# Performance work log

Hardware: AMD Instinct MI355X
Metric: run time of the kernel (lower is better)

## Reference

```python
import jax, jax.numpy as jnp
import numpy as np

N_NODES = 200000
INPUT_DIM = 128
HIDDEN_DIM = 128
NUM_WALKS = 16384   # total walks across the batch of graphs
WALK_LEN = 20


def setup_inputs() -> dict:
    key = jax.random.key(0)
    ks = jax.random.split(key, 6)
    s_in = 1.0 / np.sqrt(INPUT_DIM)
    s_h = 1.0 / np.sqrt(HIDDEN_DIM)
    return {
        "x": jax.random.normal(ks[0], (N_NODES, INPUT_DIM), dtype=jnp.float32),
        "walks": jax.random.randint(ks[1], (NUM_WALKS, WALK_LEN), 0, N_NODES),
        "W_f": jax.random.normal(ks[2], (HIDDEN_DIM, INPUT_DIM), dtype=jnp.float32) * s_in,
        "b_f": jnp.zeros((HIDDEN_DIM,), dtype=jnp.float32),
        "W_ih": jax.random.normal(ks[3], (3 * HIDDEN_DIM, HIDDEN_DIM), dtype=jnp.float32) * s_h,
        "W_hh": jax.random.normal(ks[4], (3 * HIDDEN_DIM, HIDDEN_DIM), dtype=jnp.float32) * s_h,
        "b_ih": jnp.zeros((3 * HIDDEN_DIM,), dtype=jnp.float32),
        "b_hh": jnp.zeros((3 * HIDDEN_DIM,), dtype=jnp.float32),
    }


def _gru_final(seq, W_ih, W_hh, b_ih, b_hh):
    # seq: [B, T, H]; torch GRU gate order: reset, update, new. Returns final h: [B, H].
    B = seq.shape[0]
    H = W_hh.shape[1]

    def step(h, x_t):
        gx = x_t @ W_ih.T + b_ih            # [B, 3H]
        gh = h @ W_hh.T + b_hh              # [B, 3H]
        xr, xz, xn = jnp.split(gx, 3, axis=-1)
        hr, hz, hn = jnp.split(gh, 3, axis=-1)
        r = jax.nn.sigmoid(xr + hr)
        z = jax.nn.sigmoid(xz + hz)
        n = jnp.tanh(xn + r * hn)
        h_new = (1.0 - z) * n + z * h
        return h_new, None

    h0 = jnp.zeros((B, H), dtype=seq.dtype)
    h_final, _ = jax.lax.scan(step, h0, jnp.swapaxes(seq, 0, 1))  # scan over time
    return h_final


def reference(x, walks, W_f, b_f, W_ih, W_hh, b_ih, b_hh):
    # feature_encoder: Linear(input_dim -> hidden_dim)
    x_encoded = x @ W_f.T + b_f             # [N, H]
    # vectorized replacement of the scalar double-loop gather
    walk_features = x_encoded[walks]        # [B, T, H]
    path_encodings = _gru_final(walk_features, W_ih, W_hh, b_ih, b_hh)  # [B, H]
    return path_encodings
```

## Files before the change

### kernel.cpp

```cpp
#include <hip/hip_runtime.h>
#include <cstddef>

#define NWALKS 16384
#define TLEN   20
#define HDIM   128
#define WPB    32
#define NTHR   512

typedef __attribute__((ext_vector_type(8))) _Float16 f16x8;
typedef __attribute__((ext_vector_type(4))) _Float16 f16x4;
typedef __attribute__((ext_vector_type(2))) __fp16   h16x2;
typedef __attribute__((ext_vector_type(4))) float    f32x4;

union H4 { f16x4 v; struct { h16x2 lo, hi; } p; };

__global__ void fold_kernel(const float* __restrict__ W_f, const float* __restrict__ b_f,
                            const float* __restrict__ W_ih, const float* __restrict__ W_hh,
                            const float* __restrict__ b_ih,
                            _Float16* __restrict__ Wc16, _Float16* __restrict__ Whh16,
                            float* __restrict__ b_c) {
  const int r = blockIdx.x;
  const int i = threadIdx.x;
  const float scale = (r < 256) ? -1.4426950408889634f : 2.8853900817779268f;
  const float* wih = W_ih + r * HDIM;
  float acc = 0.f;
  for (int h = 0; h < HDIM; ++h) acc = fmaf(wih[h], W_f[h * HDIM + i], acc);
  Wc16[r * HDIM + i]  = (_Float16)(acc * scale);
  Whh16[r * HDIM + i] = (_Float16)(W_hh[r * HDIM + i] * scale);
  if (i == 0) {
    float bb = b_ih[r];
    for (int h = 0; h < HDIM; ++h) bb = fmaf(wih[h], b_f[h], bb);
    b_c[r] = bb;
  }
}

__global__ __launch_bounds__(NTHR, 2)
void gru_kernel(const float* __restrict__ x, const int* __restrict__ walks,
                const _Float16* __restrict__ Wc16, const _Float16* __restrict__ Whh16,
                const float* __restrict__ b_c, const float* __restrict__ b_hh,
                float* __restrict__ out) {
  __shared__ _Float16 hbuf[2][WPB][HDIM];
  __shared__ _Float16 xbuf[2][WPB][HDIM];
  __shared__ int      nodes[TLEN][WPB];

  const int tid  = threadIdx.x;
  const int lane = tid & 63;
  const int wv   = tid >> 6;
  const int g    = lane >> 4;
  const int l15  = lane & 15;
  const int jw   = wv * 16 + l15;
  const int j0   = wv * 16 + 4 * g;
  const int walk0 = blockIdx.x * WPB;

  for (int idx = tid; idx < TLEN * WPB; idx += NTHR)
    nodes[idx >> 5][idx & 31] = walks[(walk0 + (idx & 31)) * TLEN + (idx >> 5)];
  for (int idx = tid; idx < WPB * HDIM; idx += NTHR)
    hbuf[0][0][idx] = (_Float16)0.f;

  f16x8 wrx[4], wrh[4], wzx[4], wzh[4], wnx[4], wnh[4];
#pragma unroll
  for (int kt = 0; kt < 4; ++kt) {
    const int koff = kt * 32 + g * 8;
    wrx[kt] = *(const f16x8*)(Wc16  + (size_t)(jw)       * HDIM + koff);
    wzx[kt] = *(const f16x8*)(Wc16  + (size_t)(128 + jw) * HDIM + koff);
    wnx[kt] = *(const f16x8*)(Wc16  + (size_t)(256 + jw) * HDIM + koff);
    wrh[kt] = *(const f16x8*)(Whh16 + (size_t)(jw)       * HDIM + koff);
    wzh[kt] = *(const f16x8*)(Whh16 + (size_t)(128 + jw) * HDIM + koff);
    wnh[kt] = *(const f16x8*)(Whh16 + (size_t)(256 + jw) * HDIM + koff);
  }
  const float NEG_L2E = -1.4426950408889634f;
  const float TWO_L2E =  2.8853900817779268f;
  const f32x4 br4  = NEG_L2E * (*(const f32x4*)&b_c[j0]       + *(const f32x4*)&b_hh[j0]);
  const f32x4 bz4  = NEG_L2E * (*(const f32x4*)&b_c[128 + j0] + *(const f32x4*)&b_hh[128 + j0]);
  const f32x4 bxn4 = TWO_L2E * (*(const f32x4*)&b_c[256 + j0]);
  const f32x4 bhn4 = TWO_L2E * (*(const f32x4*)&b_hh[256 + j0]);

  f32x4 hprev[2];
  hprev[0] = 0.f; hprev[1] = 0.f;

  int voffs[4];
#pragma unroll
  for (int kt = 0; kt < 4; ++kt)
    voffs[kt] = l15 * HDIM + ((((kt * 4 + g) ^ (l15 & 7))) << 3);
  const int srow = tid >> 4;
  const int sc   = tid & 15;
  const int xw   = srow * HDIM + ((sc ^ (srow & 7)) << 3);
  const int hw   = l15 * HDIM + (((2 * wv + (g >> 1)) ^ (l15 & 7)) << 3) + ((g & 1) << 2);

  __syncthreads();

  {
    const unsigned off0 = ((unsigned)nodes[0][srow] << 7) + sc * 8u;
    const f32x4 a = *(const f32x4*)(x + off0);
    const f32x4 b = *(const f32x4*)(x + off0 + 4);
    H4 lo, hi;
    lo.p.lo = __builtin_amdgcn_cvt_pkrtz(a.x, a.y);
    lo.p.hi = __builtin_amdgcn_cvt_pkrtz(a.z, a.w);
    hi.p.lo = __builtin_amdgcn_cvt_pkrtz(b.x, b.y);
    hi.p.hi = __builtin_amdgcn_cvt_pkrtz(b.z, b.w);
    *(f16x4*)(&xbuf[0][0][0] + xw)     = lo.v;
    *(f16x4*)(&xbuf[0][0][0] + xw + 4) = hi.v;
  }
  f32x4 PA0, PA1, PB0, PB1;
  {
    const unsigned off1 = ((unsigned)nodes[1][srow] << 7) + sc * 8u;
    PA0 = *(const f32x4*)(x + off1);
    PA1 = *(const f32x4*)(x + off1 + 4);
  }
  __syncthreads();

#define STEP(T, CUR, NXT, P0, P1, N0, N1)                                         \
  {                                                                               \
                             \
    const int tn = ((T) + 2 < TLEN) ? (T) + 2 : TLEN - 1;                         \
    const unsigned offn = ((unsigned)nodes[tn][srow] << 7) + sc * 8u;             \
    N0 = *(const f32x4*)(x + offn);                                               \
    N1 = *(const f32x4*)(x + offn + 4);                                           \
                                      \
    const _Float16* xb = &xbuf[CUR][0][0];                                        \
    const _Float16* hb = &hbuf[CUR][0][0];                                        \
    f32x4 ar[2], az[2], an[2], ah2[2];                                            \
    __builtin_amdgcn_s_setprio(1);                                                \
    _Pragma("unroll")                                                             \
    for (int kt = 0; kt < 4; ++kt) {                                              \
      const f16x8 ax0 = *(const f16x8*)(xb + voffs[kt]);                          \
      const f16x8 ax1 = *(const f16x8*)(xb + voffs[kt] + 16 * HDIM);              \
      const f16x8 ah0 = *(const f16x8*)(hb + voffs[kt]);                          \
      const f16x8 ah1 = *(const f16x8*)(hb + voffs[kt] + 16 * HDIM);              \
      ar[0]  = __builtin_amdgcn_mfma_f32_16x16x32_f16(wrx[kt], ax0, kt ? ar[0]  : br4,  0,0,0); \
      ar[1]  = __builtin_amdgcn_mfma_f32_16x16x32_f16(wrx[kt], ax1, kt ? ar[1]  : br4,  0,0,0); \
      ar[0]  = __builtin_amdgcn_mfma_f32_16x16x32_f16(wrh[kt], ah0, ar[0],  0,0,0); \
      ar[1]  = __builtin_amdgcn_mfma_f32_16x16x32_f16(wrh[kt], ah1, ar[1],  0,0,0); \
      az[0]  = __builtin_amdgcn_mfma_f32_16x16x32_f16(wzx[kt], ax0, kt ? az[0]  : bz4,  0,0,0); \
      az[1]  = __builtin_amdgcn_mfma_f32_16x16x32_f16(wzx[kt], ax1, kt ? az[1]  : bz4,  0,0,0); \
      az[0]  = __builtin_amdgcn_mfma_f32_16x16x32_f16(wzh[kt], ah0, az[0],  0,0,0); \
      az[1]  = __builtin_amdgcn_mfma_f32_16x16x32_f16(wzh[kt], ah1, az[1],  0,0,0); \
      an[0]  = __builtin_amdgcn_mfma_f32_16x16x32_f16(wnx[kt], ax0, kt ? an[0]  : bxn4, 0,0,0); \
      an[1]  = __builtin_amdgcn_mfma_f32_16x16x32_f16(wnx[kt], ax1, kt ? an[1]  : bxn4, 0,0,0); \
      ah2[0] = __builtin_amdgcn_mfma_f32_16x16x32_f16(wnh[kt], ah0, kt ? ah2[0] : bhn4, 0,0,0); \
      ah2[1] = __builtin_amdgcn_mfma_f32_16x16x32_f16(wnh[kt], ah1, kt ? ah2[1] : bhn4, 0,0,0); \
    }                                                                             \
    __builtin_amdgcn_s_setprio(0);                                                \
                    \
    {                                                                             \
      H4 lo, hi;                                                                  \
      lo.p.lo = __builtin_amdgcn_cvt_pkrtz(P0.x, P0.y);                           \
      lo.p.hi = __builtin_amdgcn_cvt_pkrtz(P0.z, P0.w);                           \
      hi.p.lo = __builtin_amdgcn_cvt_pkrtz(P1.x, P1.y);                           \
      hi.p.hi = __builtin_amdgcn_cvt_pkrtz(P1.z, P1.w);                           \
      *(f16x4*)(&xbuf[NXT][0][0] + xw)     = lo.v;                                \
      *(f16x4*)(&xbuf[NXT][0][0] + xw + 4) = hi.v;                                \
    }                                                                             \
                \
    _Pragma("unroll")                                                             \
    for (int mt = 0; mt < 2; ++mt) {                                              \
      f32x4 hn;                                                                   \
      _Pragma("unroll")                                                           \
      for (int r = 0; r < 4; ++r) {                                               \
        const float rv = __builtin_amdgcn_rcpf(1.f + __builtin_amdgcn_exp2f(ar[mt][r])); \
        const float zv = __builtin_amdgcn_rcpf(1.f + __builtin_amdgcn_exp2f(az[mt][r])); \
        const float en = __builtin_amdgcn_exp2f(fmaf(rv, ah2[mt][r], an[mt][r])); \
        const float nv = fmaf(-2.f, __builtin_amdgcn_rcpf(en + 1.f), 1.f);        \
        hn[r] = fmaf(zv, hprev[mt][r] - nv, nv);                                  \
      }                                                                           \
      hprev[mt] = hn;                                                             \
      H4 hp;                                                                      \
      hp.p.lo = __builtin_amdgcn_cvt_pkrtz(hn[0], hn[1]);                         \
      hp.p.hi = __builtin_amdgcn_cvt_pkrtz(hn[2], hn[3]);                         \
      *(f16x4*)(&hbuf[NXT][0][0] + hw + mt * 16 * HDIM) = hp.v;                   \
    }                                                                             \
    __syncthreads();                                                              \
  }

#pragma unroll 1
  for (int tt = 0; tt < TLEN; tt += 2) {
    STEP(tt,     0, 1, PA0, PA1, PB0, PB1)
    STEP(tt + 1, 1, 0, PB0, PB1, PA0, PA1)
  }
#undef STEP

#pragma unroll
  for (int mt = 0; mt < 2; ++mt) {
    float4 o = make_float4(hprev[mt][0], hprev[mt][1], hprev[mt][2], hprev[mt][3]);
    *(float4*)&out[(size_t)(walk0 + mt * 16 + l15) * HDIM + j0] = o;
  }
}

extern "C" void kernel_launch(void* const* d_in, const int* in_sizes, int n_in,
                              void* d_out, int out_size, void* d_ws, size_t ws_size,
                              hipStream_t stream) {
  const float* x     = (const float*)d_in[0];
  const int*   walks = (const int*)  d_in[1];
  const float* W_f   = (const float*)d_in[2];
  const float* b_f   = (const float*)d_in[3];
  const float* W_ih  = (const float*)d_in[4];
  const float* W_hh  = (const float*)d_in[5];
  const float* b_ih  = (const float*)d_in[6];
  const float* b_hh  = (const float*)d_in[7];
  float* out = (float*)d_out;

  _Float16* Wc16  = (_Float16*)d_ws;
  _Float16* Whh16 = Wc16 + 384 * HDIM;
  float*    b_c   = (float*)(Whh16 + 384 * HDIM);

  fold_kernel<<<3 * HDIM, HDIM, 0, stream>>>(W_f, b_f, W_ih, W_hh, b_ih, Wc16, Whh16, b_c);
  gru_kernel<<<NWALKS / WPB, NTHR, 0, stream>>>(x, walks, Wc16, Whh16, b_c, b_hh, out);
}
```

Baseline: 83.87 us.

## Software-pipeline GRU input projection one timestep ahead of recurrent matmul

The input-side gate projections (W_ih·x) for step t+1 are now computed during step t, after the recurrent h-projection MFMAs, and carried in registers. The critical dependent chain per step then holds only the h-side MFMAs followed by the gate math. The x prefetch distance grows to three steps, and a prologue computes step 0's x projection. This adds accumulator registers, which may raise register pressure and lower occupancy.

```diff
diff --git a/kernel.cpp b/kernel.cpp
--- a/kernel.cpp
+++ b/kernel.cpp
@@ -109,57 +109,91 @@
   }
   __syncthreads();
 
-#define STEP(T, CUR, NXT, P0, P1, N0, N1)                                         \
+  f32x4 PXRa[2], PXZa[2], PXNa[2], PXRb[2], PXZb[2], PXNb[2];
+  {
+    const _Float16* xb = &xbuf[0][0][0];
+#pragma unroll
+    for (int kt = 0; kt < 4; ++kt) {
+      const f16x8 ax0 = *(const f16x8*)(xb + voffs[kt]);
+      const f16x8 ax1 = *(const f16x8*)(xb + voffs[kt] + 16 * HDIM);
+      PXRa[0] = __builtin_amdgcn_mfma_f32_16x16x32_f16(wrx[kt], ax0, kt ? PXRa[0] : br4,  0,0,0);
+      PXRa[1] = __builtin_amdgcn_mfma_f32_16x16x32_f16(wrx[kt], ax1, kt ? PXRa[1] : br4,  0,0,0);
+      PXZa[0] = __builtin_amdgcn_mfma_f32_16x16x32_f16(wzx[kt], ax0, kt ? PXZa[0] : bz4,  0,0,0);
+      PXZa[1] = __builtin_amdgcn_mfma_f32_16x16x32_f16(wzx[kt], ax1, kt ? PXZa[1] : bz4,  0,0,0);
+      PXNa[0] = __builtin_amdgcn_mfma_f32_16x16x32_f16(wnx[kt], ax0, kt ? PXNa[0] : bxn4, 0,0,0);
+      PXNa[1] = __builtin_amdgcn_mfma_f32_16x16x32_f16(wnx[kt], ax1, kt ? PXNa[1] : bxn4, 0,0,0);
+    }
+  }
+  {
+    H4 lo, hi;
+    lo.p.lo = __builtin_amdgcn_cvt_pkrtz(PA0.x, PA0.y);
+    lo.p.hi = __builtin_amdgcn_cvt_pkrtz(PA0.z, PA0.w);
+    hi.p.lo = __builtin_amdgcn_cvt_pkrtz(PA1.x, PA1.y);
+    hi.p.hi = __builtin_amdgcn_cvt_pkrtz(PA1.z, PA1.w);
+    *(f16x4*)(&xbuf[1][0][0] + xw)     = lo.v;
+    *(f16x4*)(&xbuf[1][0][0] + xw + 4) = hi.v;
+  }
+  {
+    const unsigned off2 = ((unsigned)nodes[2][srow] << 7) + sc * 8u;
+    PB0 = *(const f32x4*)(x + off2);
+    PB1 = *(const f32x4*)(x + off2 + 4);
+  }
+  __syncthreads();
+
+#define STEP(T, XRD, XWR, HRD, HWR, L0, L1, S0, S1, PXR, PXZ, PXN, QXR, QXZ, QXN) \
   {                                                                               \
-                             \
-    const int tn = ((T) + 2 < TLEN) ? (T) + 2 : TLEN - 1;                         \
+    const int tn = ((T) + 3 < TLEN) ? (T) + 3 : TLEN - 1;                         \
     const unsigned offn = ((unsigned)nodes[tn][srow] << 7) + sc * 8u;             \
-    N0 = *(const f32x4*)(x + offn);                                               \
-    N1 = *(const f32x4*)(x + offn + 4);                                           \
-                                      \
-    const _Float16* xb = &xbuf[CUR][0][0];                                        \
-    const _Float16* hb = &hbuf[CUR][0][0];                                        \
-    f32x4 ar[2], az[2], an[2], ah2[2];                                            \
+    L0 = *(const f32x4*)(x + offn);                                               \
+    L1 = *(const f32x4*)(x + offn + 4);                                           \
+    const _Float16* xb = &xbuf[XRD][0][0];                                        \
+    const _Float16* hb = &hbuf[HRD][0][0];                                        \
+    f32x4 ah2[2];                                                                 \
     __builtin_amdgcn_s_setprio(1);                                                \
+              \
+    _Pragma("unroll")                                                             \
+    for (int kt = 0; kt < 4; ++kt) {                                              \
+      const f16x8 ah0 = *(const f16x8*)(hb + voffs[kt]);                          \
+      const f16x8 ah1 = *(const f16x8*)(hb + voffs[kt] + 16 * HDIM);              \
+      PXR[0] = __builtin_amdgcn_mfma_f32_16x16x32_f16(wrh[kt], ah0, PXR[0], 0,0,0); \
+      PXR[1] = __builtin_amdgcn_mfma_f32_16x16x32_f16(wrh[kt], ah1, PXR[1], 0,0,0); \
+      PXZ[0] = __builtin_amdgcn_mfma_f32_16x16x32_f16(wzh[kt], ah0, PXZ[0], 0,0,0); \
+      PXZ[1] = __builtin_amdgcn_mfma_f32_16x16x32_f16(wzh[kt], ah1, PXZ[1], 0,0,0); \
+      ah2[0] = __builtin_amdgcn_mfma_f32_16x16x32_f16(wnh[kt], ah0, kt ? ah2[0] : bhn4, 0,0,0); \
+      ah2[1] = __builtin_amdgcn_mfma_f32_16x16x32_f16(wnh[kt], ah1, kt ? ah2[1] : bhn4, 0,0,0); \
+    }                                                                             \
+                    \
     _Pragma("unroll")                                                             \
     for (int kt = 0; kt < 4; ++kt) {                                              \
       const f16x8 ax0 = *(const f16x8*)(xb + voffs[kt]);                          \
       const f16x8 ax1 = *(const f16x8*)(xb + voffs[kt] + 16 * HDIM);              \
-      const f16x8 ah0 = *(const f16x8*)(hb + voffs[kt]);                          \
-      const f16x8 ah1 = *(const f16x8*)(hb + voffs[kt] + 16 * HDIM);              \
-      ar[0]  = __builtin_amdgcn_mfma_f32_16x16x32_f16(wrx[kt], ax0, kt ? ar[0]  : br4,  0,0,0); \
-      ar[1]  = __builtin_amdgcn_mfma_f32_16x16x32_f16(wrx[kt], ax1, kt ? ar[1]  : br4,  0,0,0); \
-      ar[0]  = __builtin_amdgcn_mfma_f32_16x16x32_f16(wrh[kt], ah0, ar[0],  0,0,0); \
-      ar[1]  = __builtin_amdgcn_mfma_f32_16x16x32_f16(wrh[kt], ah1, ar[1],  0,0,0); \
-      az[0]  = __builtin_amdgcn_mfma_f32_16x16x32_f16(wzx[kt], ax0, kt ? az[0]  : bz4,  0,0,0); \
-      az[1]  = __builtin_amdgcn_mfma_f32_16x16x32_f16(wzx[kt], ax1, kt ? az[1]  : bz4,  0,0,0); \
-      az[0]  = __builtin_amdgcn_mfma_f32_16x16x32_f16(wzh[kt], ah0, az[0],  0,0,0); \
-      az[1]  = __builtin_amdgcn_mfma_f32_16x16x32_f16(wzh[kt], ah1, az[1],  0,0,0); \
-      an[0]  = __builtin_amdgcn_mfma_f32_16x16x32_f16(wnx[kt], ax0, kt ? an[0]  : bxn4, 0,0,0); \
-      an[1]  = __builtin_amdgcn_mfma_f32_16x16x32_f16(wnx[kt], ax1, kt ? an[1]  : bxn4, 0,0,0); \
-      ah2[0] = __builtin_amdgcn_mfma_f32_16x16x32_f16(wnh[kt], ah0, kt ? ah2[0] : bhn4, 0,0,0); \
-      ah2[1] = __builtin_amdgcn_mfma_f32_16x16x32_f16(wnh[kt], ah1, kt ? ah2[1] : bhn4, 0,0,0); \
+      QXR[0] = __builtin_amdgcn_mfma_f32_16x16x32_f16(wrx[kt], ax0, kt ? QXR[0] : br4,  0,0,0); \
+      QXR[1] = __builtin_amdgcn_mfma_f32_16x16x32_f16(wrx[kt], ax1, kt ? QXR[1] : br4,  0,0,0); \
+      QXZ[0] = __builtin_amdgcn_mfma_f32_16x16x32_f16(wzx[kt], ax0, kt ? QXZ[0] : bz4,  0,0,0); \
+      QXZ[1] = __builtin_amdgcn_mfma_f32_16x16x32_f16(wzx[kt], ax1, kt ? QXZ[1] : bz4,  0,0,0); \
+      QXN[0] = __builtin_amdgcn_mfma_f32_16x16x32_f16(wnx[kt], ax0, kt ? QXN[0] : bxn4, 0,0,0); \
+      QXN[1] = __builtin_amdgcn_mfma_f32_16x16x32_f16(wnx[kt], ax1, kt ? QXN[1] : bxn4, 0,0,0); \
     }                                                                             \
     __builtin_amdgcn_s_setprio(0);                                                \
-                    \
+                                                 \
     {                                                                             \
       H4 lo, hi;                                                                  \
-      lo.p.lo = __builtin_amdgcn_cvt_pkrtz(P0.x, P0.y);                           \
-      lo.p.hi = __builtin_amdgcn_cvt_pkrtz(P0.z, P0.w);                           \
-      hi.p.lo = __builtin_amdgcn_cvt_pkrtz(P1.x, P1.y);                           \
-      hi.p.hi = __builtin_amdgcn_cvt_pkrtz(P1.z, P1.w);                           \
-      *(f16x4*)(&xbuf[NXT][0][0] + xw)     = lo.v;                                \
-      *(f16x4*)(&xbuf[NXT][0][0] + xw + 4) = hi.v;                                \
-    }                                                                             \
-                \
+      lo.p.lo = __builtin_amdgcn_cvt_pkrtz(S0.x, S0.y);                           \
+      lo.p.hi = __builtin_amdgcn_cvt_pkrtz(S0.z, S0.w);                           \
+      hi.p.lo = __builtin_amdgcn_cvt_pkrtz(S1.x, S1.y);                           \
+      hi.p.hi = __builtin_amdgcn_cvt_pkrtz(S1.z, S1.w);                           \
+      *(f16x4*)(&xbuf[XWR][0][0] + xw)     = lo.v;                                \
+      *(f16x4*)(&xbuf[XWR][0][0] + xw + 4) = hi.v;                                \
+    }                                                                             \
+                                            \
     _Pragma("unroll")                                                             \
     for (int mt = 0; mt < 2; ++mt) {                                              \
       f32x4 hn;                                                                   \
       _Pragma("unroll")                                                           \
       for (int r = 0; r < 4; ++r) {                                               \
-        const float rv = __builtin_amdgcn_rcpf(1.f + __builtin_amdgcn_exp2f(ar[mt][r])); \
-        const float zv = __builtin_amdgcn_rcpf(1.f + __builtin_amdgcn_exp2f(az[mt][r])); \
-        const float en = __builtin_amdgcn_exp2f(fmaf(rv, ah2[mt][r], an[mt][r])); \
+        const float rv = __builtin_amdgcn_rcpf(1.f + __builtin_amdgcn_exp2f(PXR[mt][r])); \
+        const float zv = __builtin_amdgcn_rcpf(1.f + __builtin_amdgcn_exp2f(PXZ[mt][r])); \
+        const float en = __builtin_amdgcn_exp2f(fmaf(rv, ah2[mt][r], PXN[mt][r])); \
         const float nv = fmaf(-2.f, __builtin_amdgcn_rcpf(en + 1.f), 1.f);        \
         hn[r] = fmaf(zv, hprev[mt][r] - nv, nv);                                  \
       }                                                                           \
@@ -167,15 +201,15 @@
       H4 hp;                                                                      \
       hp.p.lo = __builtin_amdgcn_cvt_pkrtz(hn[0], hn[1]);                         \
       hp.p.hi = __builtin_amdgcn_cvt_pkrtz(hn[2], hn[3]);                         \
-      *(f16x4*)(&hbuf[NXT][0][0] + hw + mt * 16 * HDIM) = hp.v;                   \
+      *(f16x4*)(&hbuf[HWR][0][0] + hw + mt * 16 * HDIM) = hp.v;                   \
     }                                                                             \
     __syncthreads();                                                              \
   }
 
 #pragma unroll 1
   for (int tt = 0; tt < TLEN; tt += 2) {
-    STEP(tt,     0, 1, PA0, PA1, PB0, PB1)
-    STEP(tt + 1, 1, 0, PB0, PB1, PA0, PA1)
+    STEP(tt,     1, 0, 0, 1, PA0, PA1, PB0, PB1, PXRa, PXZa, PXNa, PXRb, PXZb, PXNb)
+    STEP(tt + 1, 0, 1, 1, 0, PB0, PB1, PA0, PA1, PXRb, PXZb, PXNb, PXRa, PXZa, PXNa)
   }
 #undef STEP
 
```

Result: slower. 87.19 us (+4.0%).

## Halve walks per block to 16 and replace syncthreads with LDS-only barrier

Applied to the files above, without the earlier changes.

Cuts walks per block from 32 to 16, so each wave handles one 16-walk MFMA tile per step instead of two. The gather, the LDS staging, the accumulators and the output write are reworked for the smaller tile. This doubles the grid to 1024 blocks and lowers register and LDS use per block, aiming for more blocks resident at once to hide gather latency and the serial recurrence. The per-step __syncthreads is replaced by an lgkmcnt wait plus s_barrier, so the outstanding global prefetch is no longer drained at each step. The cost is that every block reloads the weights into registers and each wave has less MFMA work to cover latency.

```diff
diff --git a/kernel.cpp b/kernel.cpp
--- a/kernel.cpp
+++ b/kernel.cpp
@@ -4,7 +4,7 @@
 #define NWALKS 16384
 #define TLEN   20
 #define HDIM   128
-#define WPB    32
+#define WPB    16
 #define NTHR   512
 
 typedef __attribute__((ext_vector_type(8))) _Float16 f16x8;
@@ -53,7 +53,7 @@
   const int walk0 = blockIdx.x * WPB;
 
   for (int idx = tid; idx < TLEN * WPB; idx += NTHR)
-    nodes[idx >> 5][idx & 31] = walks[(walk0 + (idx & 31)) * TLEN + (idx >> 5)];
+    nodes[idx >> 4][idx & 15] = walks[(walk0 + (idx & 15)) * TLEN + (idx >> 4)];
   for (int idx = tid; idx < WPB * HDIM; idx += NTHR)
     hbuf[0][0][idx] = (_Float16)0.f;
 
@@ -75,114 +75,99 @@
   const f32x4 bxn4 = TWO_L2E * (*(const f32x4*)&b_c[256 + j0]);
   const f32x4 bhn4 = TWO_L2E * (*(const f32x4*)&b_hh[256 + j0]);
 
-  f32x4 hprev[2];
-  hprev[0] = 0.f; hprev[1] = 0.f;
+  f32x4 hprev;
+  hprev = 0.f;
 
   int voffs[4];
 #pragma unroll
   for (int kt = 0; kt < 4; ++kt)
     voffs[kt] = l15 * HDIM + ((((kt * 4 + g) ^ (l15 & 7))) << 3);
-  const int srow = tid >> 4;
-  const int sc   = tid & 15;
-  const int xw   = srow * HDIM + ((sc ^ (srow & 7)) << 3);
+  const int srow = tid >> 5;
+  const int sc4  = tid & 31;
+  const int xw   = srow * HDIM + (((sc4 >> 1) ^ (srow & 7)) << 3) + ((sc4 & 1) << 2);
   const int hw   = l15 * HDIM + (((2 * wv + (g >> 1)) ^ (l15 & 7)) << 3) + ((g & 1) << 2);
 
   __syncthreads();
 
   {
-    const unsigned off0 = ((unsigned)nodes[0][srow] << 7) + sc * 8u;
+    const unsigned off0 = ((unsigned)nodes[0][srow] << 7) + sc4 * 4u;
     const f32x4 a = *(const f32x4*)(x + off0);
-    const f32x4 b = *(const f32x4*)(x + off0 + 4);
-    H4 lo, hi;
-    lo.p.lo = __builtin_amdgcn_cvt_pkrtz(a.x, a.y);
-    lo.p.hi = __builtin_amdgcn_cvt_pkrtz(a.z, a.w);
-    hi.p.lo = __builtin_amdgcn_cvt_pkrtz(b.x, b.y);
-    hi.p.hi = __builtin_amdgcn_cvt_pkrtz(b.z, b.w);
-    *(f16x4*)(&xbuf[0][0][0] + xw)     = lo.v;
-    *(f16x4*)(&xbuf[0][0][0] + xw + 4) = hi.v;
+    H4 v;
+    v.p.lo = __builtin_amdgcn_cvt_pkrtz(a.x, a.y);
+    v.p.hi = __builtin_amdgcn_cvt_pkrtz(a.z, a.w);
+    *(f16x4*)(&xbuf[0][0][0] + xw) = v.v;
   }
-  f32x4 PA0, PA1, PB0, PB1;
+  f32x4 PA, PB;
   {
-    const unsigned off1 = ((unsigned)nodes[1][srow] << 7) + sc * 8u;
-    PA0 = *(const f32x4*)(x + off1);
-    PA1 = *(const f32x4*)(x + off1 + 4);
+    const unsigned off1 = ((unsigned)nodes[1][srow] << 7) + sc4 * 4u;
+    PA = *(const f32x4*)(x + off1);
   }
   __syncthreads();
 
-#define STEP(T, CUR, NXT, P0, P1, N0, N1)                                         \
+#define STEP(T, CUR, NXT, P, N)                                                   \
   {                                                                               \
-                             \
+          \
     const int tn = ((T) + 2 < TLEN) ? (T) + 2 : TLEN - 1;                         \
-    const unsigned offn = ((unsigned)nodes[tn][srow] << 7) + sc * 8u;             \
-    N0 = *(const f32x4*)(x + offn);                                               \
-    N1 = *(const f32x4*)(x + offn + 4);                                           \
-                                      \
+    const unsigned offn = ((unsigned)nodes[tn][srow] << 7) + sc4 * 4u;            \
+    N = *(const f32x4*)(x + offn);                                                \
+                                   \
     const _Float16* xb = &xbuf[CUR][0][0];                                        \
     const _Float16* hb = &hbuf[CUR][0][0];                                        \
-    f32x4 ar[2], az[2], an[2], ah2[2];                                            \
+    f32x4 ar, az, an, ah2;                                                        \
     __builtin_amdgcn_s_setprio(1);                                                \
     _Pragma("unroll")                                                             \
     for (int kt = 0; kt < 4; ++kt) {                                              \
-      const f16x8 ax0 = *(const f16x8*)(xb + voffs[kt]);                          \
-      const f16x8 ax1 = *(const f16x8*)(xb + voffs[kt] + 16 * HDIM);              \
-      const f16x8 ah0 = *(const f16x8*)(hb + voffs[kt]);                          \
-      const f16x8 ah1 = *(const f16x8*)(hb + voffs[kt] + 16 * HDIM);              \
-      ar[0]  = __builtin_amdgcn_mfma_f32_16x16x32_f16(wrx[kt], ax0, kt ? ar[0]  : br4,  0,0,0); \
-      ar[1]  = __builtin_amdgcn_mfma_f32_16x16x32_f16(wrx[kt], ax1, kt ? ar[1]  : br4,  0,0,0); \
-      ar[0]  = __builtin_amdgcn_mfma_f32_16x16x32_f16(wrh[kt], ah0, ar[0],  0,0,0); \
-      ar[1]  = __builtin_amdgcn_mfma_f32_16x16x32_f16(wrh[kt], ah1, ar[1],  0,0,0); \
-      az[0]  = __builtin_amdgcn_mfma_f32_16x16x32_f16(wzx[kt], ax0, kt ? az[0]  : bz4,  0,0,0); \
-      az[1]  = __builtin_amdgcn_mfma_f32_16x16x32_f16(wzx[kt], ax1, kt ? az[1]  : bz4,  0,0,0); \
-      az[0]  = __builtin_amdgcn_mfma_f32_16x16x32_f16(wzh[kt], ah0, az[0],  0,0,0); \
-      az[1]  = __builtin_amdgcn_mfma_f32_16x16x32_f16(wzh[kt], ah1, az[1],  0,0,0); \
-      an[0]  = __builtin_amdgcn_mfma_f32_16x16x32_f16(wnx[kt], ax0, kt ? an[0]  : bxn4, 0,0,0); \
-      an[1]  = __builtin_amdgcn_mfma_f32_16x16x32_f16(wnx[kt], ax1, kt ? an[1]  : bxn4, 0,0,0); \
-      ah2[0] = __builtin_amdgcn_mfma_f32_16x16x32_f16(wnh[kt], ah0, kt ? ah2[0] : bhn4, 0,0,0); \
-      ah2[1] = __builtin_amdgcn_mfma_f32_16x16x32_f16(wnh[kt], ah1, kt ? ah2[1] : bhn4, 0,0,0); \
+      const f16x8 ax = *(const f16x8*)(xb + voffs[kt]);                           \
+      const f16x8 ah = *(const f16x8*)(hb + voffs[kt]);                           \
+      ar  = __builtin_amdgcn_mfma_f32_16x16x32_f16(wrx[kt], ax, kt ? ar  : br4,  0,0,0); \
+      ar  = __builtin_amdgcn_mfma_f32_16x16x32_f16(wrh[kt], ah, ar,  0,0,0);      \
+      az  = __builtin_amdgcn_mfma_f32_16x16x32_f16(wzx[kt], ax, kt ? az  : bz4,  0,0,0); \
+      az  = __builtin_amdgcn_mfma_f32_16x16x32_f16(wzh[kt], ah, az,  0,0,0);      \
+      an  = __builtin_amdgcn_mfma_f32_16x16x32_f16(wnx[kt], ax, kt ? an  : bxn4, 0,0,0); \
+      ah2 = __builtin_amdgcn_mfma_f32_16x16x32_f16(wnh[kt], ah, kt ? ah2 : bhn4, 0,0,0); \
     }                                                                             \
     __builtin_amdgcn_s_setprio(0);                                                \
                     \
     {                                                                             \
-      H4 lo, hi;                                                                  \
-      lo.p.lo = __builtin_amdgcn_cvt_pkrtz(P0.x, P0.y);                           \
-      lo.p.hi = __builtin_amdgcn_cvt_pkrtz(P0.z, P0.w);                           \
-      hi.p.lo = __builtin_amdgcn_cvt_pkrtz(P1.x, P1.y);                           \
-      hi.p.hi = __builtin_amdgcn_cvt_pkrtz(P1.z, P1.w);                           \
-      *(f16x4*)(&xbuf[NXT][0][0] + xw)     = lo.v;                                \
-      *(f16x4*)(&xbuf[NXT][0][0] + xw + 4) = hi.v;                                \
+      H4 v;                                                                       \
+      v.p.lo = __builtin_amdgcn_cvt_pkrtz(P.x, P.y);                              \
+      v.p.hi = __builtin_amdgcn_cvt_pkrtz(P.z, P.w);                              \
+      *(f16x4*)(&xbuf[NXT][0][0] + xw) = v.v;                                     \
     }                                                                             \
                 \
-    _Pragma("unroll")                                                             \
-    for (int mt = 0; mt < 2; ++mt) {                                              \
+    {                                                                             \
       f32x4 hn;                                                                   \
       _Pragma("unroll")                                                           \
       for (int r = 0; r < 4; ++r) {                                               \
-        const float rv = __builtin_amdgcn_rcpf(1.f + __builtin_amdgcn_exp2f(ar[mt][r])); \
-        const float zv = __builtin_amdgcn_rcpf(1.f + __builtin_amdgcn_exp2f(az[mt][r])); \
-        const float en = __builtin_amdgcn_exp2f(fmaf(rv, ah2[mt][r], an[mt][r])); \
+        const float rv = __builtin_amdgcn_rcpf(1.f + __builtin_amdgcn_exp2f(ar[r])); \
+        const float zv = __builtin_amdgcn_rcpf(1.f + __builtin_amdgcn_exp2f(az[r])); \
+        const float en = __builtin_amdgcn_exp2f(fmaf(rv, ah2[r], an[r]));         \
         const float nv = fmaf(-2.f, __builtin_amdgcn_rcpf(en + 1.f), 1.f);        \
-        hn[r] = fmaf(zv, hprev[mt][r] - nv, nv);                                  \
+        hn[r] = fmaf(zv, hprev[r] - nv, nv);                                      \
       }                                                                           \
-      hprev[mt] = hn;                                                             \
+      hprev = hn;                                                                 \
       H4 hp;                                                                      \
       hp.p.lo = __builtin_amdgcn_cvt_pkrtz(hn[0], hn[1]);                         \
       hp.p.hi = __builtin_amdgcn_cvt_pkrtz(hn[2], hn[3]);                         \
-      *(f16x4*)(&hbuf[NXT][0][0] + hw + mt * 16 * HDIM) = hp.v;                   \
+      *(f16x4*)(&hbuf[NXT][0][0] + hw) = hp.v;                                    \
     }                                                                             \
-    __syncthreads();                                                              \
+             \
+    __builtin_amdgcn_sched_barrier(0);                                            \
+    asm volatile("s_waitcnt lgkmcnt(0)" ::: "memory");                            \
+    __builtin_amdgcn_s_barrier();                                                 \
+    __builtin_amdgcn_sched_barrier(0);                                            \
   }
 
 #pragma unroll 1
   for (int tt = 0; tt < TLEN; tt += 2) {
-    STEP(tt,     0, 1, PA0, PA1, PB0, PB1)
-    STEP(tt + 1, 1, 0, PB0, PB1, PA0, PA1)
+    STEP(tt,     0, 1, PA, PB)
+    STEP(tt + 1, 1, 0, PB, PA)
   }
 #undef STEP
 
-#pragma unroll
-  for (int mt = 0; mt < 2; ++mt) {
-    float4 o = make_float4(hprev[mt][0], hprev[mt][1], hprev[mt][2], hprev[mt][3]);
-    *(float4*)&out[(size_t)(walk0 + mt * 16 + l15) * HDIM + j0] = o;
+  {
+    float4 o = make_float4(hprev[0], hprev[1], hprev[2], hprev[3]);
+    *(float4*)&out[(size_t)(walk0 + l15) * HDIM + j0] = o;
   }
 }
 
```

New measurement: 97.31 us. 1.16x slower.

## Interleave two walk groups per block to overlap MFMA with gate math

Applied to the files above, without the earlier changes.

Each block now handles 64 walks as two independent 32-walk groups, A and B, with one set of shared buffers per group. The time loop is software-pipelined so that group A's MFMA block runs while group B's gate nonlinearities and x writes run, and the reverse in the second half. Raw barriers with explicit lgkmcnt waits replace __syncthreads. The goal is to hide the transcendental and LDS latency behind matrix work, at the cost of halving blocks per CU (launch bounds 1) and adding register pressure from the duplicate accumulators. A redundant duplicate wzh load also appears in the weight loading.

```diff
diff --git a/kernel.cpp b/kernel.cpp
--- a/kernel.cpp
+++ b/kernel.cpp
@@ -4,7 +4,7 @@
 #define NWALKS 16384
 #define TLEN   20
 #define HDIM   128
-#define WPB    32
+#define WPB    64
 #define NTHR   512
 
 typedef __attribute__((ext_vector_type(8))) _Float16 f16x8;
@@ -34,14 +34,17 @@
   }
 }
 
-__global__ __launch_bounds__(NTHR, 2)
+__global__ __launch_bounds__(NTHR, 1)
 void gru_kernel(const float* __restrict__ x, const int* __restrict__ walks,
                 const _Float16* __restrict__ Wc16, const _Float16* __restrict__ Whh16,
                 const float* __restrict__ b_c, const float* __restrict__ b_hh,
                 float* __restrict__ out) {
-  __shared__ _Float16 hbuf[2][WPB][HDIM];
-  __shared__ _Float16 xbuf[2][WPB][HDIM];
-  __shared__ int      nodes[TLEN][WPB];
+  __shared__ _Float16 hbufA[32][HDIM];
+  __shared__ _Float16 xbufA[32][HDIM];
+  __shared__ _Float16 hbufB[32][HDIM];
+  __shared__ _Float16 xbufB[32][HDIM];
+  __shared__ int      nodesA[TLEN][32];
+  __shared__ int      nodesB[TLEN][32];
 
   const int tid  = threadIdx.x;
   const int lane = tid & 63;
@@ -52,10 +55,14 @@
   const int j0   = wv * 16 + 4 * g;
   const int walk0 = blockIdx.x * WPB;
 
-  for (int idx = tid; idx < TLEN * WPB; idx += NTHR)
-    nodes[idx >> 5][idx & 31] = walks[(walk0 + (idx & 31)) * TLEN + (idx >> 5)];
-  for (int idx = tid; idx < WPB * HDIM; idx += NTHR)
-    hbuf[0][0][idx] = (_Float16)0.f;
+  for (int idx = tid; idx < TLEN * 32; idx += NTHR) {
+    nodesA[idx >> 5][idx & 31] = walks[(walk0 +      (idx & 31)) * TLEN + (idx >> 5)];
+    nodesB[idx >> 5][idx & 31] = walks[(walk0 + 32 + (idx & 31)) * TLEN + (idx >> 5)];
+  }
+  for (int idx = tid; idx < 32 * HDIM; idx += NTHR) {
+    hbufA[0][idx] = (_Float16)0.f;
+    hbufB[0][idx] = (_Float16)0.f;
+  }
 
   f16x8 wrx[4], wrh[4], wzx[4], wzh[4], wnx[4], wnh[4];
 #pragma unroll
@@ -66,6 +73,7 @@
     wnx[kt] = *(const f16x8*)(Wc16  + (size_t)(256 + jw) * HDIM + koff);
     wrh[kt] = *(const f16x8*)(Whh16 + (size_t)(jw)       * HDIM + koff);
     wzh[kt] = *(const f16x8*)(Whh16 + (size_t)(128 + jw) * HDIM + koff);
+    wzh[kt] = *(const f16x8*)(Whh16 + (size_t)(128 + jw) * HDIM + koff);
     wnh[kt] = *(const f16x8*)(Whh16 + (size_t)(256 + jw) * HDIM + koff);
   }
   const float NEG_L2E = -1.4426950408889634f;
@@ -75,8 +83,9 @@
   const f32x4 bxn4 = TWO_L2E * (*(const f32x4*)&b_c[256 + j0]);
   const f32x4 bhn4 = TWO_L2E * (*(const f32x4*)&b_hh[256 + j0]);
 
-  f32x4 hprev[2];
-  hprev[0] = 0.f; hprev[1] = 0.f;
+  f32x4 hprevA[2], hprevB[2];
+  hprevA[0] = 0.f; hprevA[1] = 0.f;
+  hprevB[0] = 0.f; hprevB[1] = 0.f;
 
   int voffs[4];
 #pragma unroll
@@ -87,39 +96,53 @@
   const int xw   = srow * HDIM + ((sc ^ (srow & 7)) << 3);
   const int hw   = l15 * HDIM + (((2 * wv + (g >> 1)) ^ (l15 & 7)) << 3) + ((g & 1) << 2);
 
+  f32x4 arA[2], azA[2], anA[2], ah2A[2];
+  f32x4 arB[2], azB[2], anB[2], ah2B[2];
+  f32x4 GA0, GA1, GB0, GB1;
+
   __syncthreads();
 
   {
-    const unsigned off0 = ((unsigned)nodes[0][srow] << 7) + sc * 8u;
-    const f32x4 a = *(const f32x4*)(x + off0);
-    const f32x4 b = *(const f32x4*)(x + off0 + 4);
-    H4 lo, hi;
-    lo.p.lo = __builtin_amdgcn_cvt_pkrtz(a.x, a.y);
-    lo.p.hi = __builtin_amdgcn_cvt_pkrtz(a.z, a.w);
-    hi.p.lo = __builtin_amdgcn_cvt_pkrtz(b.x, b.y);
-    hi.p.hi = __builtin_amdgcn_cvt_pkrtz(b.z, b.w);
-    *(f16x4*)(&xbuf[0][0][0] + xw)     = lo.v;
-    *(f16x4*)(&xbuf[0][0][0] + xw + 4) = hi.v;
-  }
-  f32x4 PA0, PA1, PB0, PB1;
-  {
-    const unsigned off1 = ((unsigned)nodes[1][srow] << 7) + sc * 8u;
-    PA0 = *(const f32x4*)(x + off1);
-    PA1 = *(const f32x4*)(x + off1 + 4);
+    const unsigned offA = ((unsigned)nodesA[0][srow] << 7) + sc * 8u;
+    const unsigned offB = ((unsigned)nodesB[0][srow] << 7) + sc * 8u;
+    const f32x4 a0 = *(const f32x4*)(x + offA);
+    const f32x4 a1 = *(const f32x4*)(x + offA + 4);
+    const f32x4 b0 = *(const f32x4*)(x + offB);
+    const f32x4 b1 = *(const f32x4*)(x + offB + 4);
+    H4 va, vb, wa, wb;
+    va.p.lo = __builtin_amdgcn_cvt_pkrtz(a0.x, a0.y);
+    va.p.hi = __builtin_amdgcn_cvt_pkrtz(a0.z, a0.w);
+    vb.p.lo = __builtin_amdgcn_cvt_pkrtz(a1.x, a1.y);
+    vb.p.hi = __builtin_amdgcn_cvt_pkrtz(a1.z, a1.w);
+    wa.p.lo = __builtin_amdgcn_cvt_pkrtz(b0.x, b0.y);
+    wa.p.hi = __builtin_amdgcn_cvt_pkrtz(b0.z, b0.w);
+    wb.p.lo = __builtin_amdgcn_cvt_pkrtz(b1.x, b1.y);
+    wb.p.hi = __builtin_amdgcn_cvt_pkrtz(b1.z, b1.w);
+    *(f16x4*)(&xbufA[0][0] + xw)     = va.v;
+    *(f16x4*)(&xbufA[0][0] + xw + 4) = vb.v;
+    *(f16x4*)(&xbufB[0][0] + xw)     = wa.v;
+    *(f16x4*)(&xbufB[0][0] + xw + 4) = wb.v;
   }
   __syncthreads();
 
-#define STEP(T, CUR, NXT, P0, P1, N0, N1)                                         \
-  {                                                                               \
-                             \
-    const int tn = ((T) + 2 < TLEN) ? (T) + 2 : TLEN - 1;                         \
-    const unsigned offn = ((unsigned)nodes[tn][srow] << 7) + sc * 8u;             \
-    N0 = *(const f32x4*)(x + offn);                                               \
-    N1 = *(const f32x4*)(x + offn + 4);                                           \
-                                      \
-    const _Float16* xb = &xbuf[CUR][0][0];                                        \
-    const _Float16* hb = &hbuf[CUR][0][0];                                        \
-    f32x4 ar[2], az[2], an[2], ah2[2];                                            \
+#define RAWBAR()                                                                  \
+  __builtin_amdgcn_sched_barrier(0);                                              \
+  asm volatile("s_waitcnt lgkmcnt(0)" ::: "memory");                              \
+  __builtin_amdgcn_s_barrier();                                                   \
+  __builtin_amdgcn_sched_barrier(0);
+
+#define GATHER(nodesP, T, G0, G1)                                                 \
+  {                                                                               \
+    const int tn = ((T) < TLEN) ? (T) : TLEN - 1;                                 \
+    const unsigned o = ((unsigned)nodesP[tn][srow] << 7) + sc * 8u;               \
+    G0 = *(const f32x4*)(x + o);                                                  \
+    G1 = *(const f32x4*)(x + o + 4);                                              \
+  }
+
+#define MFMA_BLOCK(xbufP, hbufP, ar, az, an, ah2)                                 \
+  {                                                                               \
+    const _Float16* xb = &xbufP[0][0];                                            \
+    const _Float16* hb = &hbufP[0][0];                                            \
     __builtin_amdgcn_s_setprio(1);                                                \
     _Pragma("unroll")                                                             \
     for (int kt = 0; kt < 4; ++kt) {                                              \
@@ -141,17 +164,10 @@
       ah2[1] = __builtin_amdgcn_mfma_f32_16x16x32_f16(wnh[kt], ah1, kt ? ah2[1] : bhn4, 0,0,0); \
     }                                                                             \
     __builtin_amdgcn_s_setprio(0);                                                \
-                    \
-    {                                                                             \
-      H4 lo, hi;                                                                  \
-      lo.p.lo = __builtin_amdgcn_cvt_pkrtz(P0.x, P0.y);                           \
-      lo.p.hi = __builtin_amdgcn_cvt_pkrtz(P0.z, P0.w);                           \
-      hi.p.lo = __builtin_amdgcn_cvt_pkrtz(P1.x, P1.y);                           \
-      hi.p.hi = __builtin_amdgcn_cvt_pkrtz(P1.z, P1.w);                           \
-      *(f16x4*)(&xbuf[NXT][0][0] + xw)     = lo.v;                                \
-      *(f16x4*)(&xbuf[NXT][0][0] + xw + 4) = hi.v;                                \
-    }                                                                             \
-                \
+  }
+
+#define GATES(ar, az, an, ah2, hprevP, hbufP)                                     \
+  {                                                                               \
     _Pragma("unroll")                                                             \
     for (int mt = 0; mt < 2; ++mt) {                                              \
       f32x4 hn;                                                                   \
@@ -161,28 +177,56 @@
         const float zv = __builtin_amdgcn_rcpf(1.f + __builtin_amdgcn_exp2f(az[mt][r])); \
         const float en = __builtin_amdgcn_exp2f(fmaf(rv, ah2[mt][r], an[mt][r])); \
         const float nv = fmaf(-2.f, __builtin_amdgcn_rcpf(en + 1.f), 1.f);        \
-        hn[r] = fmaf(zv, hprev[mt][r] - nv, nv);                                  \
+        hn[r] = fmaf(zv, hprevP[mt][r] - nv, nv);                                 \
       }                                                                           \
-      hprev[mt] = hn;                                                             \
+      hprevP[mt] = hn;                                                            \
       H4 hp;                                                                      \
       hp.p.lo = __builtin_amdgcn_cvt_pkrtz(hn[0], hn[1]);                         \
       hp.p.hi = __builtin_amdgcn_cvt_pkrtz(hn[2], hn[3]);                         \
-      *(f16x4*)(&hbuf[NXT][0][0] + hw + mt * 16 * HDIM) = hp.v;                   \
+      *(f16x4*)(&hbufP[0][0] + hw + mt * 16 * HDIM) = hp.v;                       \
     }                                                                             \
-    __syncthreads();                                                              \
+  }
+
+#define XWRITE(xbufP, G0, G1)                                                     \
+  {                                                                               \
+    H4 lo, hi;                                                                    \
+    lo.p.lo = __builtin_amdgcn_cvt_pkrtz(G0.x, G0.y);                             \
+    lo.p.hi = __builtin_amdgcn_cvt_pkrtz(G0.z, G0.w);                             \
+    hi.p.lo = __builtin_amdgcn_cvt_pkrtz(G1.x, G1.y);                             \
+    hi.p.hi = __builtin_amdgcn_cvt_pkrtz(G1.z, G1.w);                             \
+    *(f16x4*)(&xbufP[0][0] + xw)     = lo.v;                                      \
+    *(f16x4*)(&xbufP[0][0] + xw + 4) = hi.v;                                      \
   }
 
 #pragma unroll 1
-  for (int tt = 0; tt < TLEN; tt += 2) {
-    STEP(tt,     0, 1, PA0, PA1, PB0, PB1)
-    STEP(tt + 1, 1, 0, PB0, PB1, PA0, PA1)
-  }
-#undef STEP
+  for (int k = 0; k < TLEN; ++k) {
+    GATHER(nodesA, k + 1, GA0, GA1)
+    MFMA_BLOCK(xbufA, hbufA, arA, azA, anA, ah2A)
+    if (k > 0) {
+      GATES(arB, azB, anB, ah2B, hprevB, hbufB)
+      XWRITE(xbufB, GB0, GB1)
+    }
+    RAWBAR()
+    GATHER(nodesB, k + 1, GB0, GB1)
+    MFMA_BLOCK(xbufB, hbufB, arB, azB, anB, ah2B)
+    GATES(arA, azA, anA, ah2A, hprevA, hbufA)
+    XWRITE(xbufA, GA0, GA1)
+    RAWBAR()
+  }
+  GATES(arB, azB, anB, ah2B, hprevB, hbufB)
+
+#undef RAWBAR
+#undef GATHER
+#undef MFMA_BLOCK
+#undef GATES
+#undef XWRITE
 
 #pragma unroll
   for (int mt = 0; mt < 2; ++mt) {
-    float4 o = make_float4(hprev[mt][0], hprev[mt][1], hprev[mt][2], hprev[mt][3]);
-    *(float4*)&out[(size_t)(walk0 + mt * 16 + l15) * HDIM + j0] = o;
+    float4 oa = make_float4(hprevA[mt][0], hprevA[mt][1], hprevA[mt][2], hprevA[mt][3]);
+    float4 ob = make_float4(hprevB[mt][0], hprevB[mt][1], hprevB[mt][2], hprevB[mt][3]);
+    *(float4*)&out[(size_t)(walk0 +      mt * 16 + l15) * HDIM + j0] = oa;
+    *(float4*)&out[(size_t)(walk0 + 32 + mt * 16 + l15) * HDIM + j0] = ob;
   }
 }
 
```

Measured after the change: 80.34 us. 1.04x faster.
